# Performance work log

Hardware: AMD Instinct MI355X
Metric: run time of the kernel (lower is better)

The kernel has to match this reference:

```python
import jax, jax.numpy as jnp
import numpy as np

B, C, W, F, NC = 512, 12, 4, 512, 4  # batch, leads, windows(=4, hardcoded by conv0), features, classes


def setup_inputs() -> dict:
    key = jax.random.key(0)
    ks = jax.random.split(key, 16)
    g = lambda i, shape, s=1.0: jax.random.normal(ks[i], shape, jnp.float32) * s
    return {
        "x": g(0, (B, C, W, F)),
        # GRU (PyTorch layout: W_ih [3F,F], W_hh [3F,F], gate order r,z,n)
        "gru_wih": g(1, (3 * F, F), 0.03),
        "gru_whh": g(2, (3 * F, F), 0.03),
        "gru_bih": jnp.zeros((3 * F,), jnp.float32),
        "gru_bhh": jnp.zeros((3 * F,), jnp.float32),
        # GraphLearning 1x1 convs (squeezed kernels); positive biases keep adj nondegenerate
        "conv0_w": g(3, (W,), 0.5), "conv0_b": jnp.float32(0.1),
        "conv1_w": g(4, (F,), 0.05), "conv1_b": jnp.float32(0.1),
        "conv2_w": g(5, (C * C, C), 0.3),
        "conv2_b": 0.1 + 0.05 * jnp.abs(g(6, (C * C,))),
        # GCN stack
        "gcn_w": g(7, (2, F, F), 0.04), "gcn_b": jnp.zeros((2, F), jnp.float32),
        # classifier head (jax [in,out] layout); BN in eval mode
        "fc1_w": g(8, (C * F, 512), 0.02), "fc1_b": jnp.zeros((512,), jnp.float32),
        "bn1_g": jnp.ones((512,), jnp.float32), "bn1_b": jnp.zeros((512,), jnp.float32),
        "bn1_m": 0.1 * g(9, (512,)), "bn1_v": 1.0 + 0.1 * jnp.abs(g(10, (512,))),
        "fc2_w": g(11, (512, 512), 0.04), "fc2_b": jnp.zeros((512,), jnp.float32),
        "bn2_g": jnp.ones((512,), jnp.float32), "bn2_b": jnp.zeros((512,), jnp.float32),
        "bn2_m": 0.1 * g(12, (512,)), "bn2_v": 1.0 + 0.1 * jnp.abs(g(13, (512,))),
        "fc3_w": g(14, (512, NC), 0.04), "fc3_b": jnp.zeros((NC,), jnp.float32),
    }


def reference(x, gru_wih, gru_whh, gru_bih, gru_bhh,
              conv0_w, conv0_b, conv1_w, conv1_b, conv2_w, conv2_b,
              gcn_w, gcn_b,
              fc1_w, fc1_b, bn1_g, bn1_b, bn1_m, bn1_v,
              fc2_w, fc2_b, bn2_g, bn2_b, bn2_m, bn2_v,
              fc3_w, fc3_b):
    b, c, w, f = x.shape
    # --- GRU over leads dim; each window slice starts from h0=0, so merge (batch, w) ---
    xs = x.transpose(0, 2, 1, 3).reshape(b * w, c, f)            # [N, C, F]
    xW = jnp.einsum('ntf,gf->ntg', xs, gru_wih) + gru_bih        # precompute input gates [N,C,3F]

    def step(h, xw_t):
        hg = h @ gru_whh.T + gru_bhh
        xr, xz, xn = jnp.split(xw_t, 3, axis=-1)
        hr, hz, hn = jnp.split(hg, 3, axis=-1)
        r = jax.nn.sigmoid(xr + hr)
        z = jax.nn.sigmoid(xz + hz)
        n = jnp.tanh(xn + r * hn)
        h = (1.0 - z) * n + z * h
        return h, h

    _, hs = jax.lax.scan(step, jnp.zeros((b * w, f), x.dtype), xW.transpose(1, 0, 2))
    gru_out = hs.transpose(1, 0, 2).reshape(b, w, c, f).transpose(0, 2, 1, 3)  # [B,C,W,F]

    # --- GraphLearning: 1x1 convs -> 12x12 adjacency -> normalized Laplacian -> Chebyshev K=4 ---
    g0 = gru_out.transpose(0, 2, 1, 3)                               # [B,W,C,F]
    y = jax.nn.relu(jnp.einsum('bwcf,w->bcf', g0, conv0_w) + conv0_b)  # [B,C,F]
    y = jax.nn.relu(jnp.einsum('bcf,f->bc', y, conv1_w) + conv1_b)     # [B,C]
    y = jax.nn.relu(jnp.einsum('bc,kc->bk', y, conv2_w) + conv2_b)     # [B,C*C]
    a = jnp.mean(y.reshape(b, c, c), axis=0)
    adj = jax.nn.relu(a)
    degree = jnp.sum(adj, axis=1)
    adj_s = 0.5 * (adj + adj.T)
    d_hat = 1.0 / (jnp.sqrt(degree) + 1e-7)
    lap = d_hat[:, None] * (jnp.diag(degree) - adj_s) * d_hat[None, :]
    L0 = jnp.zeros_like(lap)
    L1 = lap
    L2 = 2.0 * lap @ L1 - L0
    L3 = 2.0 * lap @ L2 - L1
    cheb = jnp.stack([L0, L1, L2, L3], axis=0)                       # [4,C,C]

    # --- GCN stack with residuals (dropout is identity in eval) ---
    h = gru_out.transpose(0, 2, 1, 3)[:, :, None]                    # [B,W,1,C,F]
    tmp = h
    res = h
    for i in range(gcn_w.shape[0]):
        support = jnp.einsum('bwocf,fg->bwocg', h, gcn_w[i])
        out = jnp.einsum('wij,bwojf->bwoif', cheb, support) + gcn_b[i]
        h = jax.nn.relu(out) + res
        res = h
    h = tmp + h
    h = h[:, :, 0].sum(1).reshape(b, c * f)                          # [B, C*F]

    # --- classifier head (eval-mode BN, dropout identity) ---
    def bn(v, gmm, bt, m, var):
        return (v - m) / jnp.sqrt(var + 1e-5) * gmm + bt

    h = bn(jax.nn.leaky_relu(h @ fc1_w + fc1_b, 0.01), bn1_g, bn1_b, bn1_m, bn1_v)
    h = bn(jax.nn.leaky_relu(h @ fc2_w + fc2_b, 0.01), bn2_g, bn2_b, bn2_m, bn2_v)
    return h @ fc3_w + fc3_b
```

## Files before the change

kernel.cpp:

```cpp
#include <hip/hip_runtime.h>
#include <cmath>

constexpr int Bb  = 512;
constexpr int Cc  = 12;
constexpr int Ww  = 4;
constexpr int Ff  = 512;
constexpr int Mx  = Bb * Ww * Cc;

typedef __attribute__((ext_vector_type(8))) short bf16x8;
typedef __attribute__((ext_vector_type(4))) float f32x4;

__device__ __forceinline__ float sigm(float v) { return 1.f / (1.f + expf(-v)); }
__device__ __forceinline__ float b2f(ushort u) { union { float f; unsigned i; } v; v.i = ((unsigned)u) << 16; return v.f; }
__device__ __forceinline__ ushort f2b(float f) {
    union { float f; unsigned i; } v; v.f = f;
    unsigned r = v.i + 0x7FFFu + ((v.i >> 16) & 1u);
    return (ushort)(r >> 16);
}
__device__ __forceinline__ void async16(const ushort* g, ushort* l) {
    __builtin_amdgcn_global_load_lds(
        (const __attribute__((address_space(1))) unsigned int*)g,
        (__attribute__((address_space(3))) unsigned int*)l, 16, 0, 0);
}

__global__ __launch_bounds__(256) void mfma_gemm(
    const ushort* __restrict__ A, const ushort* __restrict__ Bt,
    float* __restrict__ Cf, ushort* __restrict__ Cb,
    const float* __restrict__ colBias,
    int N, int K, int kLen, int MN, int gridY)
{
    __shared__ ushort As[128 * 64], Bs[128 * 64];
    const int tid = threadIdx.x;
    const int ln = tid & 63, wv = tid >> 6;
    const int l = blockIdx.x;
    const int by = l % gridY, bx = l / gridY, bz = blockIdx.y;
    const int srow = ln >> 3;
    const int kslot = (ln & 7) ^ srow;
    const int rowA0 = by * 128 + wv * 32;
    const int rowB0 = bx * 128 + wv * 32;
    const ushort* ga = A  + (long)(rowA0 + srow) * K + bz * kLen + kslot * 8;
    const ushort* gb = Bt + (long)(rowB0 + srow) * K + bz * kLen + kslot * 8;
    ushort* la = As + wv * 32 * 64;
    ushort* lb = Bs + wv * 32 * 64;
    const int rbase = (wv >> 1) * 64, cbase = (wv & 1) * 64;
    const int mrow = ln & 15, quad = ln >> 4;

    f32x4 acc[4][4] = {};

    for (int kc = 0; kc < kLen; kc += 64) {
        #pragma unroll
        for (int i = 0; i < 4; ++i) {
            async16(ga + (long)(i * 8) * K, la + i * 8 * 64);
            async16(gb + (long)(i * 8) * K, lb + i * 8 * 64);
        }
        ga += 64; gb += 64;
        __syncthreads();
        #pragma unroll
        for (int s = 0; s < 2; ++s) {
            const int sw = (((s << 2) + quad) ^ (ln & 7)) << 3;
            bf16x8 af[4], bf[4];
            #pragma unroll
            for (int i = 0; i < 4; ++i)
                af[i] = *(const bf16x8*)(As + (rbase + i * 16 + mrow) * 64 + sw);
            #pragma unroll
            for (int j = 0; j < 4; ++j)
                bf[j] = *(const bf16x8*)(Bs + (cbase + j * 16 + mrow) * 64 + sw);
            #pragma unroll
            for (int i = 0; i < 4; ++i)
                #pragma unroll
                for (int j = 0; j < 4; ++j)
                    acc[i][j] = __builtin_amdgcn_mfma_f32_16x16x32_bf16(bf[j], af[i], acc[i][j], 0, 0, 0);
        }
        __syncthreads();
    }

    const int gr0 = by * 128 + rbase + mrow;
    const int gc0 = bx * 128 + cbase + quad * 4;
    if (Cb) {
        #pragma unroll
        for (int i = 0; i < 4; ++i) {
            const long rowoff = (long)(gr0 + i * 16) * N;
            #pragma unroll
            for (int j = 0; j < 4; ++j) {
                float c0 = 0.f, c1 = 0.f, c2 = 0.f, c3 = 0.f;
                if (colBias) {
                    const float4 cb4 = *(const float4*)(colBias + gc0 + j * 16);
                    c0 = cb4.x; c1 = cb4.y; c2 = cb4.z; c3 = cb4.w;
                }
                union { ushort u[4]; uint2 v; } pk;
                pk.u[0] = f2b(acc[i][j][0] + c0);
                pk.u[1] = f2b(acc[i][j][1] + c1);
                pk.u[2] = f2b(acc[i][j][2] + c2);
                pk.u[3] = f2b(acc[i][j][3] + c3);
                *(uint2*)&Cb[rowoff + gc0 + j * 16] = pk.v;
            }
        }
    } else {
        float* Co = Cf + (long)bz * MN;
        #pragma unroll
        for (int i = 0; i < 4; ++i) {
            const long rowoff = (long)(gr0 + i * 16) * N;
            #pragma unroll
            for (int j = 0; j < 4; ++j)
                *(f32x4*)&Co[rowoff + gc0 + j * 16] = acc[i][j];
        }
    }
}

__global__ __launch_bounds__(512, 1) void gru_persist(
    const ushort* __restrict__ xW, const ushort* __restrict__ whhB,
    const float* __restrict__ bih, const float* __restrict__ bhh,
    ushort* __restrict__ h0, ushort* __restrict__ h1,
    ushort* __restrict__ G, unsigned* __restrict__ bar)
{
    __shared__ ushort Bw[8 * 96 * 64];
    __shared__ ushort Ah[2][128 * 64];
    const int tid = threadIdx.x, ln = tid & 63, wv = tid >> 6;
    const int mb = blockIdx.x & 15, fb = blockIdx.x >> 4;
    const int srow = ln >> 3, kslot = (ln & 7) ^ srow;
    const int mrow = ln & 15, quad = ln >> 4;

    #pragma unroll
    for (int i = 0; i < 12; ++i) {
        const int rg = i * 8 + wv;
        const int kc6 = rg / 12, rgi = rg - kc6 * 12;
        const int r0 = rgi * 8, r = r0 + srow;
        const int g = r >> 5, fc = r & 31;
        async16(whhB + (long)(g * 512 + fb * 32 + fc) * 512 + kc6 * 64 + kslot * 8,
                Bw + (kc6 * 96 + r0) * 64);
    }

    float br[2][4], bz[2][4], bni[2][4], bnh[2][4];
    #pragma unroll
    for (int ft = 0; ft < 2; ++ft) {
        const int f0 = fb * 32 + ft * 16 + quad * 4;
        const float4 bir = *(const float4*)(bih + f0);
        const float4 biz = *(const float4*)(bih + 512 + f0);
        const float4 bin = *(const float4*)(bih + 1024 + f0);
        const float4 bhr = *(const float4*)(bhh + f0);
        const float4 bhz = *(const float4*)(bhh + 512 + f0);
        const float4 bhn = *(const float4*)(bhh + 1024 + f0);
        br[ft][0] = bir.x + bhr.x; br[ft][1] = bir.y + bhr.y; br[ft][2] = bir.z + bhr.z; br[ft][3] = bir.w + bhr.w;
        bz[ft][0] = biz.x + bhz.x; bz[ft][1] = biz.y + bhz.y; bz[ft][2] = biz.z + bhz.z; bz[ft][3] = biz.w + bhz.w;
        bni[ft][0] = bin.x; bni[ft][1] = bin.y; bni[ft][2] = bin.z; bni[ft][3] = bin.w;
        bnh[ft][0] = bhn.x; bnh[ft][1] = bhn.y; bnh[ft][2] = bhn.z; bnh[ft][3] = bhn.w;
    }
    __syncthreads();

    const int n = mb * 128 + wv * 16 + mrow;
    unsigned* cptr = bar + mb * 16;

    const int st0 = (mb * 256 + (wv * 16 + fb) * 2 + 0) * 256 + (mrow * 4 + quad) * 4;
    const int st1 = st0 + 256;

    const int u1 = tid + 512;
    const int awv0 = tid >> 7, afbi0 = (tid >> 6) & 1, aft0 = (tid >> 5) & 1, aj0 = tid & 31;
    const int awv1 = u1 >> 7,  afbi1 = (u1 >> 6) & 1,  aft1 = (u1 >> 5) & 1,  aj1 = u1 & 31;
    const int ar0 = awv0 * 16 + (aj0 >> 1);
    const int ac0 = ((afbi0 * 4 + aft0 * 2 + (aj0 & 1)) ^ (ar0 & 7));
    const int ad0 = ar0 * 64 + ac0 * 8;
    const int ar1 = awv1 * 16 + (aj1 >> 1);
    const int ac1 = ((afbi1 * 4 + aft1 * 2 + (aj1 & 1)) ^ (ar1 & 7));
    const int ad1 = ar1 * 64 + ac1 * 8;
    const int ag0 = mb * 65536 + ((awv0 * 16 + afbi0) * 2 + aft0) * 256 + aj0 * 8;
    const int ag1 = mb * 65536 + ((awv1 * 16 + afbi1) * 2 + aft1) * 256 + aj1 * 8;

    uint2 hprev[2]; hprev[0].x = 0u; hprev[0].y = 0u; hprev[1] = hprev[0];

    for (int t = 0; t < 12; ++t) {
        const ushort* hin = (t & 1) ? h1 : h0;
        ushort* hout = (t & 1) ? h0 : h1;
        f32x4 acc[6] = {};

        const long xrow = ((long)n * 12 + t) * 1536;
        uint2 xrv[2], xzv[2], xnv[2];
        #pragma unroll
        for (int ft = 0; ft < 2; ++ft) {
            const int f0 = fb * 32 + ft * 16 + quad * 4;
            xrv[ft] = *(const uint2*)(xW + xrow + f0);
            xzv[ft] = *(const uint2*)(xW + xrow + 512 + f0);
            xnv[ft] = *(const uint2*)(xW + xrow + 1024 + f0);
        }

        if (t > 0) {
            unsigned long long ha[8][2][2];
            #pragma unroll
            for (int kc = 0; kc < 8; ++kc) {
                const ushort* p0 = hin + ag0 + kc * 1024;
                const ushort* p1 = hin + ag1 + kc * 1024;
                ha[kc][0][0] = __hip_atomic_load((const unsigned long long*)p0,
                                                 __ATOMIC_RELAXED, __HIP_MEMORY_SCOPE_AGENT);
                ha[kc][0][1] = __hip_atomic_load((const unsigned long long*)(p0 + 4),
                                                 __ATOMIC_RELAXED, __HIP_MEMORY_SCOPE_AGENT);
                ha[kc][1][0] = __hip_atomic_load((const unsigned long long*)p1,
                                                 __ATOMIC_RELAXED, __HIP_MEMORY_SCOPE_AGENT);
                ha[kc][1][1] = __hip_atomic_load((const unsigned long long*)(p1 + 4),
                                                 __ATOMIC_RELAXED, __HIP_MEMORY_SCOPE_AGENT);
            }
            {
                ulonglong2 v0; v0.x = ha[0][0][0]; v0.y = ha[0][0][1];
                ulonglong2 v1; v1.x = ha[0][1][0]; v1.y = ha[0][1][1];
                *(ulonglong2*)(Ah[0] + ad0) = v0;
                *(ulonglong2*)(Ah[0] + ad1) = v1;
            }
            __syncthreads();
            #pragma unroll
            for (int kc = 0; kc < 8; ++kc) {
                if (kc < 7) {
                    ulonglong2 v0; v0.x = ha[kc + 1][0][0]; v0.y = ha[kc + 1][0][1];
                    ulonglong2 v1; v1.x = ha[kc + 1][1][0]; v1.y = ha[kc + 1][1][1];
                    *(ulonglong2*)(Ah[(kc + 1) & 1] + ad0) = v0;
                    *(ulonglong2*)(Ah[(kc + 1) & 1] + ad1) = v1;
                }
                const ushort* Bk = Bw + kc * (96 * 64);
                const ushort* Ak = Ah[kc & 1];
                #pragma unroll
                for (int s = 0; s < 2; ++s) {
                    const int sw = (((s << 2) + quad) ^ (ln & 7)) << 3;
                    const bf16x8 ah = *(const bf16x8*)(Ak + (wv * 16 + mrow) * 64 + sw);
                    #pragma unroll
                    for (int jt = 0; jt < 6; ++jt) {
                        const bf16x8 bh = *(const bf16x8*)(Bk + (jt * 16 + mrow) * 64 + sw);
                        acc[jt] = __builtin_amdgcn_mfma_f32_16x16x32_bf16(bh, ah, acc[jt], 0, 0, 0);
                    }
                }
                __syncthreads();
            }
        }

        #pragma unroll
        for (int ft = 0; ft < 2; ++ft) {
            const ushort* xr = (const ushort*)&xrv[ft];
            const ushort* xz = (const ushort*)&xzv[ft];
            const ushort* xn = (const ushort*)&xnv[ft];
            const ushort* hp = (const ushort*)&hprev[ft];
            union { ushort u[4]; uint2 v; } o;
            #pragma unroll
            for (int r = 0; r < 4; ++r) {
                const float rr = sigm(acc[ft][r] + b2f(xr[r]) + br[ft][r]);
                const float zz = sigm(acc[2 + ft][r] + b2f(xz[r]) + bz[ft][r]);
                const float nv = tanhf(b2f(xn[r]) + bni[ft][r] + rr * (acc[4 + ft][r] + bnh[ft][r]));
                o.u[r] = f2b((1.f - zz) * nv + zz * b2f(hp[r]));
            }
            hprev[ft] = o.v;
        }

        if (t < 11) {
            union { uint2 v; unsigned long long q; } q0, q1;
            q0.v = hprev[0]; q1.v = hprev[1];
            __hip_atomic_store((unsigned long long*)&hout[st0], q0.q,
                               __ATOMIC_RELAXED, __HIP_MEMORY_SCOPE_AGENT);
            __hip_atomic_store((unsigned long long*)&hout[st1], q1.q,
                               __ATOMIC_RELAXED, __HIP_MEMORY_SCOPE_AGENT);
            asm volatile("s_waitcnt vmcnt(0)" ::: "memory");
            __syncthreads();
            if (tid == 0)
                __hip_atomic_fetch_add(cptr, 1u, __ATOMIC_RELAXED, __HIP_MEMORY_SCOPE_AGENT);
        }

        {
            const int f0 = fb * 32 + quad * 4;
            *(uint2*)&G[((long)n * 12 + t) * 512 + f0] = hprev[0];
            *(uint2*)&G[((long)n * 12 + t) * 512 + f0 + 16] = hprev[1];
        }

        if (t < 11) {
            if (tid == 0) {
                const unsigned tgt = (unsigned)(t + 1) * 16u;
                while (__hip_atomic_load(cptr, __ATOMIC_RELAXED, __HIP_MEMORY_SCOPE_AGENT) < tgt)
                    __builtin_amdgcn_s_sleep(1);
            }
            __syncthreads();
        }
    }
}

__global__ __launch_bounds__(256) void cvt_x(const float* __restrict__ x, ushort* __restrict__ xb)
{
    const int idx = blockIdx.x * 256 + threadIdx.x;
    const int m = idx >> 6, f8 = (idx & 63) << 3;
    const int n = m / 12, c = m - n * 12;
    const int b = n >> 2, w = n & 3;
    const float* src = x + (((b * 12 + c) * 4 + w) << 9) + f8;
    const float4 a = *(const float4*)src, q = *(const float4*)(src + 4);
    uint4 o;
    o.x = (unsigned)f2b(a.x) | ((unsigned)f2b(a.y) << 16);
    o.y = (unsigned)f2b(a.z) | ((unsigned)f2b(a.w) << 16);
    o.z = (unsigned)f2b(q.x) | ((unsigned)f2b(q.y) << 16);
    o.w = (unsigned)f2b(q.z) | ((unsigned)f2b(q.w) << 16);
    *(uint4*)(xb + (m << 9) + f8) = o;
}

__global__ __launch_bounds__(256) void cvt_w2(
    const float* __restrict__ wih, const float* __restrict__ whh,
    ushort* __restrict__ wihB, ushort* __restrict__ whhB)
{
    int bx = blockIdx.x;
    const float* s; ushort* d;
    if (bx < 384) { s = wih; d = wihB; } else { s = whh; d = whhB; bx -= 384; }
    const int e = (bx * 256 + threadIdx.x) << 3;
    const float4 a = *(const float4*)(s + e), q = *(const float4*)(s + e + 4);
    uint4 o;
    o.x = (unsigned)f2b(a.x) | ((unsigned)f2b(a.y) << 16);
    o.y = (unsigned)f2b(a.z) | ((unsigned)f2b(a.w) << 16);
    o.z = (unsigned)f2b(q.x) | ((unsigned)f2b(q.y) << 16);
    o.w = (unsigned)f2b(q.z) | ((unsigned)f2b(q.w) << 16);
    *(uint4*)(d + e) = o;
}

__global__ __launch_bounds__(256) void tcvt_all(
    const float* __restrict__ gcnw, const float* __restrict__ f1w, const float* __restrict__ f2w,
    ushort* __restrict__ gw0, ushort* __restrict__ gw1,
    ushort* __restrict__ f1t, ushort* __restrict__ f2t)
{
    int by = blockIdx.y;
    const float* src; ushort* dst; int R, C;
    if (by < 16)       { src = gcnw;          dst = gw0; R = 512;  C = 512; }
    else if (by < 32)  { src = gcnw + 262144; dst = gw1; R = 512;  C = 512; by -= 16; }
    else if (by < 224) { src = f1w;           dst = f1t; R = 6144; C = 512; by -= 32; }
    else               { src = f2w;           dst = f2t; R = 512;  C = 512; by -= 224; }
    __shared__ float tl[32][33];
    const int c0 = blockIdx.x * 32, r0 = by * 32;
    const int cx = threadIdx.x & 31, ry = threadIdx.x >> 5;
    #pragma unroll
    for (int k = 0; k < 4; ++k) tl[ry + k * 8][cx] = src[(long)(r0 + ry + k * 8) * C + c0 + cx];
    __syncthreads();
    #pragma unroll
    for (int k = 0; k < 4; ++k) dst[(long)(c0 + ry + k * 8) * R + r0 + cx] = f2b(tl[cx][ry + k * 8]);
}

__global__ __launch_bounds__(256) void conv01(
    const ushort* __restrict__ G, const float* __restrict__ w0, const float* __restrict__ b0,
    const float* __restrict__ w1, const float* __restrict__ b1, float* __restrict__ y2)
{
    const int row = (blockIdx.x * 256 + threadIdx.x) >> 6;
    const int lane = threadIdx.x & 63;
    const int b = row / 12, c = row - 12 * b;
    const float w00 = w0[0], w01 = w0[1], w02 = w0[2], w03 = w0[3], bb = b0[0];
    const ushort* gp = G + ((long)(b * 4) * 12 + c) * 512;
    float s = 0.f;
    for (int f = lane; f < 512; f += 64) {
        const float v = bb + b2f(gp[f]) * w00 + b2f(gp[6144 + f]) * w01
                      + b2f(gp[12288 + f]) * w02 + b2f(gp[18432 + f]) * w03;
        s += fmaxf(v, 0.f) * w1[f];
    }
    #pragma unroll
    for (int off = 32; off; off >>= 1) s += __shfl_down(s, off);
    if (lane == 0) y2[row] = fmaxf(s + b1[0], 0.f);
}

__global__ __launch_bounds__(256) void conv2_cheb(
    const float* __restrict__ y2, const float* __restrict__ w2,
    const float* __restrict__ b2, float* __restrict__ cheb)
{
    __shared__ float ys[6144];
    __shared__ float adj[144], deg[12], dhat[12], lap[144], T2[144];
    const int tid = threadIdx.x;
    for (int i = tid; i < 6144; i += 256) ys[i] = y2[i];
    __syncthreads();
    if (tid < 144) {
        float wk[12];
        #pragma unroll
        for (int c = 0; c < 12; ++c) wk[c] = w2[tid * 12 + c];
        const float bias = b2[tid];
        float s = 0.f;
        for (int b = 0; b < 512; ++b) {
            float v = bias;
            #pragma unroll
            for (int c = 0; c < 12; ++c) v += ys[b * 12 + c] * wk[c];
            s += fmaxf(v, 0.f);
        }
        adj[tid] = fmaxf(s * (1.f / 512.f), 0.f);
    }
    __syncthreads();
    if (tid < 12) {
        float s = 0.f;
        for (int j = 0; j < 12; ++j) s += adj[tid * 12 + j];
        deg[tid] = s; dhat[tid] = 1.f / (sqrtf(s) + 1e-7f);
    }
    __syncthreads();
    if (tid < 144) {
        const int i = tid / 12, j = tid % 12;
        const float as = 0.5f * (adj[i * 12 + j] + adj[j * 12 + i]);
        lap[tid] = dhat[i] * ((i == j ? deg[i] : 0.f) - as) * dhat[j];
    }
    __syncthreads();
    if (tid < 144) {
        const int i = tid / 12, j = tid % 12;
        float s = 0.f;
        for (int kk = 0; kk < 12; ++kk) s += lap[i * 12 + kk] * lap[kk * 12 + j];
        T2[tid] = 2.f * s;
    }
    __syncthreads();
    if (tid < 144) {
        const int i = tid / 12, j = tid % 12;
        float s = 0.f;
        for (int kk = 0; kk < 12; ++kk) s += lap[i * 12 + kk] * T2[kk * 12 + j];
        cheb[tid] = 0.f;
        cheb[144 + tid] = lap[tid];
        cheb[288 + tid] = T2[tid];
        cheb[432 + tid] = 2.f * s - lap[tid];
    }
}

__global__ __launch_bounds__(256) void gcn_epi1(
    const ushort* __restrict__ S, const float* __restrict__ cheb,
    const float* __restrict__ gcnb, const ushort* __restrict__ G,
    ushort* __restrict__ H1)
{
    __shared__ float ch[576];
    const int tid = threadIdx.x;
    for (int i = tid; i < 576; i += 256) ch[i] = cheb[i];
    __syncthreads();
    const int idx = blockIdx.x * 256 + tid;
    const int f = idx & 511, bc = idx >> 9;
    const int b = bc / 12, c = bc - 12 * b;
    const float bias = gcnb[f];
    #pragma unroll
    for (int w = 0; w < 4; ++w) {
        float o = bias;
        const ushort* Sr = S + ((b * 4 + w) * 12) * 512 + f;
        const float* cw = ch + w * 144 + c * 12;
        #pragma unroll
        for (int j = 0; j < 12; ++j) o += cw[j] * b2f(Sr[j * 512]);
        const int gi = ((b * 4 + w) * 12 + c) * 512 + f;
        H1[gi] = f2b(fmaxf(o, 0.f) + b2f(G[gi]));
    }
}

__global__ __launch_bounds__(256) void gcn_epi2(
    const ushort* __restrict__ S, const float* __restrict__ cheb,
    const float* __restrict__ gcnb, const ushort* __restrict__ G,
    const ushort* __restrict__ H1, ushort* __restrict__ pooled)
{
    __shared__ float ch[576];
    const int tid = threadIdx.x;
    for (int i = tid; i < 576; i += 256) ch[i] = cheb[i];
    __syncthreads();
    const int idx = blockIdx.x * 256 + tid;
    const int f = idx & 511, bc = idx >> 9;
    const int b = bc / 12, c = bc - 12 * b;
    const float bias = gcnb[f];
    float acc = 0.f;
    #pragma unroll
    for (int w = 0; w < 4; ++w) {
        float o = bias;
        const ushort* Sr = S + ((b * 4 + w) * 12) * 512 + f;
        const float* cw = ch + w * 144 + c * 12;
        #pragma unroll
        for (int j = 0; j < 12; ++j) o += cw[j] * b2f(Sr[j * 512]);
        const int gi = ((b * 4 + w) * 12 + c) * 512 + f;
        acc += fmaxf(o, 0.f) + b2f(H1[gi]) + b2f(G[gi]);
    }
    pooled[idx] = f2b(acc);
}

__global__ __launch_bounds__(256) void fc_epi(
    const float* __restrict__ part, int nsplit, const float* __restrict__ bias,
    const float* __restrict__ g, const float* __restrict__ be,
    const float* __restrict__ mu, const float* __restrict__ var,
    ushort* __restrict__ outb, float* __restrict__ outf)
{
    const int idx = blockIdx.x * 256 + threadIdx.x;
    const int c = idx & 511;
    float s = bias[c];
    for (int k = 0; k < nsplit; ++k) s += part[k * 262144 + idx];
    s = s >= 0.f ? s : 0.01f * s;
    s = (s - mu[c]) * rsqrtf(var[c] + 1e-5f) * g[c] + be[c];
    if (outb) outb[idx] = f2b(s); else outf[idx] = s;
}

__global__ __launch_bounds__(256) void fc3_kernel(
    const float* __restrict__ z2, const float* __restrict__ w3,
    const float* __restrict__ b3, float* __restrict__ out)
{
    const int idx = blockIdx.x * 256 + threadIdx.x;
    const int m = idx >> 2, nc = idx & 3;
    float s = b3[nc];
    const float* zr = z2 + m * 512;
    for (int k = 0; k < 512; ++k) s += zr[k] * w3[k * 4 + nc];
    out[idx] = s;
}

extern "C" void kernel_launch(void* const* d_in, const int* in_sizes, int n_in,
                              void* d_out, int out_size, void* d_ws, size_t ws_size,
                              hipStream_t stream)
{
    (void)in_sizes; (void)n_in; (void)out_size; (void)ws_size;
    const float* x    = (const float*)d_in[0];
    const float* wih  = (const float*)d_in[1];
    const float* whh  = (const float*)d_in[2];
    const float* bih  = (const float*)d_in[3];
    const float* bhh  = (const float*)d_in[4];
    const float* c0w  = (const float*)d_in[5];
    const float* c0b  = (const float*)d_in[6];
    const float* c1w  = (const float*)d_in[7];
    const float* c1b  = (const float*)d_in[8];
    const float* c2w  = (const float*)d_in[9];
    const float* c2b  = (const float*)d_in[10];
    const float* gcnw = (const float*)d_in[11];
    const float* gcnb = (const float*)d_in[12];
    const float* f1w  = (const float*)d_in[13];
    const float* f1b  = (const float*)d_in[14];
    const float* bn1g = (const float*)d_in[15];
    const float* bn1b = (const float*)d_in[16];
    const float* bn1m = (const float*)d_in[17];
    const float* bn1v = (const float*)d_in[18];
    const float* f2w  = (const float*)d_in[19];
    const float* f2b_ = (const float*)d_in[20];
    const float* bn2g = (const float*)d_in[21];
    const float* bn2b = (const float*)d_in[22];
    const float* bn2m = (const float*)d_in[23];
    const float* bn2v = (const float*)d_in[24];
    const float* f3w  = (const float*)d_in[25];
    const float* f3b  = (const float*)d_in[26];

    char* W = (char*)d_ws;
    ushort* xW     = (ushort*)(W + 0);
    ushort* S      = (ushort*)(W + 0);
    ushort* H1     = (ushort*)(W + 25165824);
    ushort* pooled = (ushort*)(W + 50331648);
    float*  z1p    = (float*)(W + 58720256);
    float*  z2p    = z1p;
    ushort* xb     = (ushort*)(W + 75497472);
    ushort* G      = (ushort*)(W + 75497472);
    ushort* h0     = (ushort*)(W + 100663296);
    ushort* h1     = (ushort*)(W + 102760448);
    ushort* whhB   = (ushort*)(W + 104857600);
    ushort* wihB   = (ushort*)(W + 106430464);
    ushort* gw0    = (ushort*)(W + 108003328);
    ushort* gw1    = (ushort*)(W + 108527616);
    ushort* f1t    = (ushort*)(W + 109051904);
    ushort* f2t    = (ushort*)(W + 115343360);
    ushort* z1b    = (ushort*)(W + 115867648);
    float*  z2     = (float*)(W + 116391936);
    float*  y2     = (float*)(W + 117440512);
    float*  chebb  = (float*)(W + 117465088);
    unsigned* bar  = (unsigned*)(W + 117467392);

    hipMemsetAsync(bar, 0, 1024, stream);
    cvt_x<<<(Mx * 64) / 256, 256, 0, stream>>>(x, xb);
    cvt_w2<<<768, 256, 0, stream>>>(wih, whh, wihB, whhB);
    tcvt_all<<<dim3(16, 240), 256, 0, stream>>>(gcnw, f1w, f2w, gw0, gw1, f1t, f2t);

    mfma_gemm<<<dim3(2304, 1), 256, 0, stream>>>(
        xb, wihB, nullptr, xW, nullptr, 3 * Ff, Ff, Ff, 0, 192);
    gru_persist<<<256, 512, 0, stream>>>(xW, whhB, bih, bhh, h0, h1, G, bar);

    conv01<<<(Bb * Cc * 64) / 256, 256, 0, stream>>>(G, c0w, c0b, c1w, c1b, y2);
    conv2_cheb<<<1, 256, 0, stream>>>(y2, c2w, c2b, chebb);

    mfma_gemm<<<dim3(768, 1), 256, 0, stream>>>(
        G, gw0, nullptr, S, nullptr, Ff, Ff, Ff, 0, 192);
    gcn_epi1<<<(Bb * Cc * Ff) / 256, 256, 0, stream>>>(S, chebb, gcnb, G, H1);

    mfma_gemm<<<dim3(768, 1), 256, 0, stream>>>(
        H1, gw1, nullptr, S, nullptr, Ff, Ff, Ff, 0, 192);
    gcn_epi2<<<(Bb * Cc * Ff) / 256, 256, 0, stream>>>(S, chebb, gcnb + Ff, G, H1, pooled);

    mfma_gemm<<<dim3(16, 16), 256, 0, stream>>>(
        pooled, f1t, z1p, nullptr, nullptr, 512, Cc * Ff, 384, 262144, 4);
    fc_epi<<<1024, 256, 0, stream>>>(z1p, 16, f1b, bn1g, bn1b, bn1m, bn1v, z1b, nullptr);
    mfma_gemm<<<dim3(16, 4), 256, 0, stream>>>(
        z1b, f2t, z2p, nullptr, nullptr, 512, 512, 128, 262144, 4);
    fc_epi<<<1024, 256, 0, stream>>>(z2p, 4, f2b_, bn2g, bn2b, bn2m, bn2v, nullptr, z2);
    fc3_kernel<<<(Bb * 4) / 256, 256, 0, stream>>>(z2, f3w, f3b, (float*)d_out);
}
```

Before: 518.7 us.

## Load GRU hidden state directly into MFMA fragment registers, dropping LDS staging

Result: faster. 493.4 us (-4.9%).

```diff
diff --git a/kernel.cpp b/kernel.cpp
--- a/kernel.cpp
+++ b/kernel.cpp
@@ -114,7 +114,6 @@
     ushort* __restrict__ G, unsigned* __restrict__ bar)
 {
     __shared__ ushort Bw[8 * 96 * 64];
-    __shared__ ushort Ah[2][128 * 64];
     const int tid = threadIdx.x, ln = tid & 63, wv = tid >> 6;
     const int mb = blockIdx.x & 15, fb = blockIdx.x >> 4;
     const int srow = ln >> 3, kslot = (ln & 7) ^ srow;
@@ -150,20 +149,9 @@
     const int n = mb * 128 + wv * 16 + mrow;
     unsigned* cptr = bar + mb * 16;
 
-    const int st0 = (mb * 256 + (wv * 16 + fb) * 2 + 0) * 256 + (mrow * 4 + quad) * 4;
-    const int st1 = st0 + 256;
-
-    const int u1 = tid + 512;
-    const int awv0 = tid >> 7, afbi0 = (tid >> 6) & 1, aft0 = (tid >> 5) & 1, aj0 = tid & 31;
-    const int awv1 = u1 >> 7,  afbi1 = (u1 >> 6) & 1,  aft1 = (u1 >> 5) & 1,  aj1 = u1 & 31;
-    const int ar0 = awv0 * 16 + (aj0 >> 1);
-    const int ac0 = ((afbi0 * 4 + aft0 * 2 + (aj0 & 1)) ^ (ar0 & 7));
-    const int ad0 = ar0 * 64 + ac0 * 8;
-    const int ar1 = awv1 * 16 + (aj1 >> 1);
-    const int ac1 = ((afbi1 * 4 + aft1 * 2 + (aj1 & 1)) ^ (ar1 & 7));
-    const int ad1 = ar1 * 64 + ac1 * 8;
-    const int ag0 = mb * 65536 + ((awv0 * 16 + afbi0) * 2 + aft0) * 256 + aj0 * 8;
-    const int ag1 = mb * 65536 + ((awv1 * 16 + afbi1) * 2 + aft1) * 256 + aj1 * 8;
+    const int rbase0 = ((mb * 8 + wv) * 16) * 512;
+    const int aoff = (quad >> 1) * 256 + mrow * 16 + (quad & 1) * 8;
+    const int sbase = ((mb * 8 + wv) * 16 + fb) * 512 + mrow * 16 + quad * 4;
 
     uint2 hprev[2]; hprev[0].x = 0u; hprev[0].y = 0u; hprev[1] = hprev[0];
 
@@ -171,6 +159,18 @@
         const ushort* hin = (t & 1) ? h1 : h0;
         ushort* hout = (t & 1) ? h0 : h1;
         f32x4 acc[6] = {};
+
+        unsigned long long ha[16][2];
+        if (t > 0) {
+            #pragma unroll
+            for (int sl = 0; sl < 16; ++sl) {
+                const ushort* p = hin + rbase0 + sl * 512 + aoff;
+                ha[sl][0] = __hip_atomic_load((const unsigned long long*)p,
+                                              __ATOMIC_RELAXED, __HIP_MEMORY_SCOPE_AGENT);
+                ha[sl][1] = __hip_atomic_load((const unsigned long long*)(p + 4),
+                                              __ATOMIC_RELAXED, __HIP_MEMORY_SCOPE_AGENT);
+            }
+        }
 
         const long xrow = ((long)n * 12 + t) * 1536;
         uint2 xrv[2], xzv[2], xnv[2];
@@ -183,48 +183,21 @@
         }
 
         if (t > 0) {
-            unsigned long long ha[8][2][2];
             #pragma unroll
             for (int kc = 0; kc < 8; ++kc) {
-                const ushort* p0 = hin + ag0 + kc * 1024;
-                const ushort* p1 = hin + ag1 + kc * 1024;
-                ha[kc][0][0] = __hip_atomic_load((const unsigned long long*)p0,
-                                                 __ATOMIC_RELAXED, __HIP_MEMORY_SCOPE_AGENT);
-                ha[kc][0][1] = __hip_atomic_load((const unsigned long long*)(p0 + 4),
-                                                 __ATOMIC_RELAXED, __HIP_MEMORY_SCOPE_AGENT);
-                ha[kc][1][0] = __hip_atomic_load((const unsigned long long*)p1,
-                                                 __ATOMIC_RELAXED, __HIP_MEMORY_SCOPE_AGENT);
-                ha[kc][1][1] = __hip_atomic_load((const unsigned long long*)(p1 + 4),
-                                                 __ATOMIC_RELAXED, __HIP_MEMORY_SCOPE_AGENT);
-            }
-            {
-                ulonglong2 v0; v0.x = ha[0][0][0]; v0.y = ha[0][0][1];
-                ulonglong2 v1; v1.x = ha[0][1][0]; v1.y = ha[0][1][1];
-                *(ulonglong2*)(Ah[0] + ad0) = v0;
-                *(ulonglong2*)(Ah[0] + ad1) = v1;
-            }
-            __syncthreads();
-            #pragma unroll
-            for (int kc = 0; kc < 8; ++kc) {
-                if (kc < 7) {
-                    ulonglong2 v0; v0.x = ha[kc + 1][0][0]; v0.y = ha[kc + 1][0][1];
-                    ulonglong2 v1; v1.x = ha[kc + 1][1][0]; v1.y = ha[kc + 1][1][1];
-                    *(ulonglong2*)(Ah[(kc + 1) & 1] + ad0) = v0;
-                    *(ulonglong2*)(Ah[(kc + 1) & 1] + ad1) = v1;
-                }
                 const ushort* Bk = Bw + kc * (96 * 64);
-                const ushort* Ak = Ah[kc & 1];
                 #pragma unroll
                 for (int s = 0; s < 2; ++s) {
+                    union { unsigned long long q[2]; bf16x8 v; } af;
+                    af.q[0] = ha[kc * 2 + s][0];
+                    af.q[1] = ha[kc * 2 + s][1];
                     const int sw = (((s << 2) + quad) ^ (ln & 7)) << 3;
-                    const bf16x8 ah = *(const bf16x8*)(Ak + (wv * 16 + mrow) * 64 + sw);
                     #pragma unroll
                     for (int jt = 0; jt < 6; ++jt) {
                         const bf16x8 bh = *(const bf16x8*)(Bk + (jt * 16 + mrow) * 64 + sw);
-                        acc[jt] = __builtin_amdgcn_mfma_f32_16x16x32_bf16(bh, ah, acc[jt], 0, 0, 0);
+                        acc[jt] = __builtin_amdgcn_mfma_f32_16x16x32_bf16(bh, af.v, acc[jt], 0, 0, 0);
                     }
                 }
-                __syncthreads();
             }
         }
 
@@ -248,9 +221,9 @@
         if (t < 11) {
             union { uint2 v; unsigned long long q; } q0, q1;
             q0.v = hprev[0]; q1.v = hprev[1];
-            __hip_atomic_store((unsigned long long*)&hout[st0], q0.q,
+            __hip_atomic_store((unsigned long long*)&hout[sbase], q0.q,
                                __ATOMIC_RELAXED, __HIP_MEMORY_SCOPE_AGENT);
-            __hip_atomic_store((unsigned long long*)&hout[st1], q1.q,
+            __hip_atomic_store((unsigned long long*)&hout[sbase + 256], q1.q,
                                __ATOMIC_RELAXED, __HIP_MEMORY_SCOPE_AGENT);
             asm volatile("s_waitcnt vmcnt(0)" ::: "memory");
             __syncthreads();
```
